# Optimization experiments

Measured on AMD Instinct MI355X. Metric: run time of the kernel, lower is better.

The kernel has to match this reference:

```python
import jax, jax.numpy as jnp
import numpy as np

B, H, N, D = 2, 16, 4096, 128
SCALE = 1.0


def setup_inputs() -> dict:
    key = jax.random.key(0)
    kq, kk, kv, kg = jax.random.split(key, 4)
    shape = (B, H, N, D)
    return {
        "q": jax.random.normal(kq, shape, dtype=jnp.float32),
        "k": jax.random.normal(kk, shape, dtype=jnp.float32),
        "v": jax.random.normal(kv, shape, dtype=jnp.float32),
        "g": jax.random.normal(kg, shape, dtype=jnp.float32),
    }


def reference(q, k, v, g):
    # FLAOperator(mode='gla') CPU fallback: gla_scan
    # recurrence: s_t = s_{t-1} + sigmoid(q_t*k_t + g_t) * v_t ; y_t = s_t
    qs = q * SCALE
    # move time axis (N) to the front for lax.scan: [N, B, H, D]
    seq = tuple(jnp.moveaxis(t, 2, 0) for t in (qs, k, v, g))
    s0 = jnp.zeros((q.shape[0], q.shape[1], q.shape[3]), dtype=q.dtype)  # [B, H, D]

    def step(s, xs):
        q_t, k_t, v_t, g_t = xs
        s = s + jax.nn.sigmoid(q_t * k_t + g_t) * v_t
        return s, s

    _, y = jax.lax.scan(step, s0, seq)  # y: [N, B, H, D]
    return jnp.moveaxis(y, 0, 2)  # [B, H, N, D]
```

## Files before the change

### kernel.cpp

```cpp
#include <hip/hip_runtime.h>
#include <math.h>

static constexpr int kN   = 4096;
static constexpr int kD   = 128;
static constexpr int kBH  = 32;
static constexpr int kD4  = 32;

typedef float  v4f __attribute__((ext_vector_type(4)));

__device__ __forceinline__ float fast_sigmoid(float x) {
    return __builtin_amdgcn_rcpf(1.0f + __expf(-x));
}

__device__ __forceinline__ unsigned short f2b(float x) {
    union { float f; unsigned u; } cv; cv.f = x;
    unsigned u = cv.u;
    u += 0x7fffu + ((u >> 16) & 1u);
    return (unsigned short)(u >> 16);
}
__device__ __forceinline__ float b2f(unsigned short b) {
    union { unsigned u; float f; } cv; cv.u = ((unsigned)b) << 16;
    return cv.f;
}

static constexpr int C1 = 512;
static constexpr int T1 = kN / C1;
static constexpr int TASKS1 = kBH * C1;

__global__ __launch_bounds__(256) void gla1_scan(
    const float4* __restrict__ q, const float4* __restrict__ k,
    const float4* __restrict__ v, const float4* __restrict__ g,
    ushort4* __restrict__ wscan, float4* __restrict__ sums)
{
    const int gtid = blockIdx.x * 256 + threadIdx.x;
    const int lane = gtid & (kD4 - 1);
    const int task = gtid >> 5;
    const int bh   = task >> 9;
    const int c    = task & (C1 - 1);

    const size_t base = ((size_t)bh * kN + (size_t)c * T1) * kD4 + lane;
    float4 acc = make_float4(0.f, 0.f, 0.f, 0.f);
#pragma unroll
    for (int t = 0; t < T1; ++t) {
        const size_t idx = base + (size_t)t * kD4;
        const float4 q4 = q[idx];
        const float4 k4 = k[idx];
        const float4 g4 = g[idx];
        const float4 v4 = v[idx];
        acc.x += v4.x * fast_sigmoid(q4.x * k4.x + g4.x);
        acc.y += v4.y * fast_sigmoid(q4.y * k4.y + g4.y);
        acc.z += v4.z * fast_sigmoid(q4.z * k4.z + g4.z);
        acc.w += v4.w * fast_sigmoid(q4.w * k4.w + g4.w);
        ushort4 p;
        p.x = f2b(acc.x); p.y = f2b(acc.y); p.z = f2b(acc.z); p.w = f2b(acc.w);
        wscan[idx] = p;
    }
    sums[(size_t)task * kD4 + lane] = acc;
}

__global__ void gla1_chunkscan(float* __restrict__ sums)
{
    const int bh = blockIdx.x;
    const int d  = threadIdx.x;
    const size_t base = (size_t)bh * C1 * kD + d;
    float run = 0.f;
    for (int c0 = 0; c0 < C1; c0 += 8) {
        float tv[8];
#pragma unroll
        for (int j = 0; j < 8; ++j)
            tv[j] = sums[base + (size_t)(c0 + j) * kD];
#pragma unroll
        for (int j = 0; j < 8; ++j) {
            const float t = tv[j];
            sums[base + (size_t)(c0 + j) * kD] = run;
            run += t;
        }
    }
}

__global__ __launch_bounds__(256) void gla1_emit(
    const ushort4* __restrict__ wscan, const float4* __restrict__ sums,
    float4* __restrict__ out)
{
    const int gtid = blockIdx.x * 256 + threadIdx.x;
    const int lane = gtid & (kD4 - 1);
    const int task = gtid >> 5;
    const int bh   = task >> 9;
    const int c    = task & (C1 - 1);

    const float4 pre = sums[(size_t)task * kD4 + lane];
    const size_t base = ((size_t)bh * kN + (size_t)c * T1) * kD4 + lane;
#pragma unroll
    for (int t = 0; t < T1; ++t) {
        const size_t idx = base + (size_t)t * kD4;
        const ushort4 p = wscan[idx];
        v4f o;
        o.x = b2f(p.x) + pre.x;
        o.y = b2f(p.y) + pre.y;
        o.z = b2f(p.z) + pre.z;
        o.w = b2f(p.w) + pre.w;
        __builtin_nontemporal_store(o, (v4f*)&out[idx]);
    }
}

template <int CC>
__global__ __launch_bounds__(256) void gla_pass1(
    const float4* __restrict__ q, const float4* __restrict__ k,
    const float4* __restrict__ v, const float4* __restrict__ g,
    float4* __restrict__ out, float4* __restrict__ sums)
{
    constexpr int TT = kN / CC;
    const int gtid = blockIdx.x * 256 + threadIdx.x;
    const int lane = gtid & (kD4 - 1);
    const int task = gtid >> 5;
    const int bh   = task / CC;
    const int c    = task & (CC - 1);
    size_t base = ((size_t)bh * kN + (size_t)c * TT) * kD4 + lane;
    float4 acc = make_float4(0.f, 0.f, 0.f, 0.f);
#pragma unroll 4
    for (int t = 0; t < TT; ++t) {
        const size_t idx = base + (size_t)t * kD4;
        const float4 q4 = q[idx], k4 = k[idx], g4 = g[idx], v4 = v[idx];
        acc.x += v4.x * fast_sigmoid(q4.x * k4.x + g4.x);
        acc.y += v4.y * fast_sigmoid(q4.y * k4.y + g4.y);
        acc.z += v4.z * fast_sigmoid(q4.z * k4.z + g4.z);
        acc.w += v4.w * fast_sigmoid(q4.w * k4.w + g4.w);
        out[idx] = acc;
    }
    sums[(size_t)task * kD4 + lane] = acc;
}

template <int CC>
__global__ void gla_pass2(float* __restrict__ sums)
{
    const int bh = blockIdx.x;
    const int d  = threadIdx.x;
    size_t base = (size_t)bh * CC * kD + d;
    float run = 0.f;
#pragma unroll
    for (int c2 = 0; c2 < CC; ++c2) {
        const size_t i = base + (size_t)c2 * kD;
        const float t = sums[i];
        sums[i] = run;
        run += t;
    }
}

template <int CC>
__global__ __launch_bounds__(256) void gla_pass3(
    float4* __restrict__ out, const float4* __restrict__ sums)
{
    constexpr int TT = kN / CC;
    const int gtid = blockIdx.x * 256 + threadIdx.x;
    const int lane = gtid & (kD4 - 1);
    const int nt   = gtid >> 5;
    const int bh   = nt / kN;
    const int t    = nt & (kN - 1);
    const int c    = t / TT;
    const float4 add = sums[((size_t)bh * CC + c) * kD4 + lane];
    float4 o = out[gtid];
    o.x += add.x; o.y += add.y; o.z += add.z; o.w += add.w;
    out[gtid] = o;
}

extern "C" void kernel_launch(void* const* d_in, const int* in_sizes, int n_in,
                              void* d_out, int out_size, void* d_ws,
                              size_t ws_size, hipStream_t stream)
{
    const float4* q = (const float4*)d_in[0];
    const float4* k = (const float4*)d_in[1];
    const float4* v = (const float4*)d_in[2];
    const float4* g = (const float4*)d_in[3];
    float4* out = (float4*)d_out;

    constexpr size_t kWscanBytes = (size_t)kBH * kN * kD4 * sizeof(ushort4);
    constexpr size_t kSumsBytes  = (size_t)TASKS1 * kD4 * sizeof(float4);
    constexpr size_t kNeed1 = kWscanBytes + kSumsBytes;

    if (ws_size >= kNeed1) {
        ushort4* wscan = (ushort4*)d_ws;
        float4*  sums  = (float4*)((char*)d_ws + kWscanBytes);
        const int blocks = TASKS1 * 32 / 256;
        gla1_scan<<<blocks, 256, 0, stream>>>(q, k, v, g, wscan, sums);
        gla1_chunkscan<<<kBH, kD, 0, stream>>>((float*)sums);
        gla1_emit<<<blocks, 256, 0, stream>>>(wscan, sums, out);
    } else if (ws_size >= (size_t)kBH * 128 * kD * sizeof(float)) {
        constexpr int CC = 128;
        const int threads1 = kBH * CC * 32;
        gla_pass1<CC><<<threads1 / 256, 256, 0, stream>>>(q, k, v, g, out,
                                                          (float4*)d_ws);
        gla_pass2<CC><<<kBH, kD, 0, stream>>>((float*)d_ws);
        const int threads3 = kBH * kN * kD4;
        gla_pass3<CC><<<threads3 / 256, 256, 0, stream>>>(out,
                                                          (const float4*)d_ws);
    } else {
        constexpr int CC = 32;
        const int threads1 = kBH * CC * 32;
        gla_pass1<CC><<<threads1 / 256, 256, 0, stream>>>(q, k, v, g, out,
                                                          (float4*)d_ws);
        gla_pass2<CC><<<kBH, kD, 0, stream>>>((float*)d_ws);
        const int threads3 = kBH * kN * kD4;
        gla_pass3<CC><<<threads3 / 256, 256, 0, stream>>>(out,
                                                          (const float4*)d_ws);
    }
}
```

Baseline: 81.55 us.

## Replace serial chunk-sum scan with hierarchical block-reduced macro scan

The scan kernel now also reduces its 8 chunk sums per block through shared memory into a per-block macro sum. A short 64-step macro scan and a new parallel per-block prefix kernel replace the old 512-step serial chunk scan that ran on only 32 blocks. The emit kernel also preloads all of its bf16 partials before storing. This shortens the serial critical path but adds one extra kernel launch, a __syncthreads, and a small amount of extra workspace traffic.

```diff
diff --git a/kernel.cpp b/kernel.cpp
--- a/kernel.cpp
+++ b/kernel.cpp
@@ -26,19 +26,25 @@
 static constexpr int C1 = 512;
 static constexpr int T1 = kN / C1;
 static constexpr int TASKS1 = kBH * C1;
+static constexpr int M1 = 64;
 
 __global__ __launch_bounds__(256) void gla1_scan(
     const float4* __restrict__ q, const float4* __restrict__ k,
     const float4* __restrict__ v, const float4* __restrict__ g,
-    ushort4* __restrict__ wscan, float4* __restrict__ sums)
-{
+    ushort4* __restrict__ wscan, float4* __restrict__ sums,
+    float4* __restrict__ macros)
+{
+    __shared__ float4 lds[8][kD4];
+
     const int gtid = blockIdx.x * 256 + threadIdx.x;
     const int lane = gtid & (kD4 - 1);
     const int task = gtid >> 5;
     const int bh   = task >> 9;
     const int c    = task & (C1 - 1);
+    const int grp  = threadIdx.x >> 5;
 
     const size_t base = ((size_t)bh * kN + (size_t)c * T1) * kD4 + lane;
+
     float4 acc = make_float4(0.f, 0.f, 0.f, 0.f);
 #pragma unroll
     for (int t = 0; t < T1; ++t) {
@@ -56,25 +62,59 @@
         wscan[idx] = p;
     }
     sums[(size_t)task * kD4 + lane] = acc;
-}
-
-__global__ void gla1_chunkscan(float* __restrict__ sums)
+    lds[grp][lane] = acc;
+    __syncthreads();
+
+    if (threadIdx.x < kD4) {
+        float4 s = lds[0][threadIdx.x];
+#pragma unroll
+        for (int g2 = 1; g2 < 8; ++g2) {
+            const float4 a = lds[g2][threadIdx.x];
+            s.x += a.x; s.y += a.y; s.z += a.z; s.w += a.w;
+        }
+        macros[(size_t)blockIdx.x * kD4 + threadIdx.x] = s;
+    }
+}
+
+__global__ void gla1_macroscan(float* __restrict__ M)
 {
     const int bh = blockIdx.x;
     const int d  = threadIdx.x;
-    const size_t base = (size_t)bh * C1 * kD + d;
+    const size_t base = (size_t)bh * M1 * kD + d;
     float run = 0.f;
-    for (int c0 = 0; c0 < C1; c0 += 8) {
-        float tv[8];
-#pragma unroll
-        for (int j = 0; j < 8; ++j)
-            tv[j] = sums[base + (size_t)(c0 + j) * kD];
-#pragma unroll
-        for (int j = 0; j < 8; ++j) {
+    for (int m0 = 0; m0 < M1; m0 += 16) {
+        float tv[16];
+#pragma unroll
+        for (int j = 0; j < 16; ++j)
+            tv[j] = M[base + (size_t)(m0 + j) * kD];
+#pragma unroll
+        for (int j = 0; j < 16; ++j) {
             const float t = tv[j];
-            sums[base + (size_t)(c0 + j) * kD] = run;
+            M[base + (size_t)(m0 + j) * kD] = run;
             run += t;
         }
+    }
+}
+
+__global__ __launch_bounds__(128) void gla1_chunkpre(
+    float* __restrict__ S, const float* __restrict__ M)
+{
+    const int b  = blockIdx.x;
+    const int d  = threadIdx.x;
+    const int bh = b >> 6;
+    const int m  = b & (M1 - 1);
+    const size_t sbase = ((size_t)bh * C1 + (size_t)m * 8) * kD + d;
+
+    float r[8];
+#pragma unroll
+    for (int j = 0; j < 8; ++j)
+        r[j] = S[sbase + (size_t)j * kD];
+    float pre = M[(size_t)b * kD + d];
+#pragma unroll
+    for (int j = 0; j < 8; ++j) {
+        const float t = r[j];
+        S[sbase + (size_t)j * kD] = pre;
+        pre += t;
     }
 }
 
@@ -88,18 +128,22 @@
     const int bh   = task >> 9;
     const int c    = task & (C1 - 1);
 
+    const size_t base = ((size_t)bh * kN + (size_t)c * T1) * kD4 + lane;
+
+    ushort4 p[T1];
+#pragma unroll
+    for (int t = 0; t < T1; ++t)
+        p[t] = wscan[base + (size_t)t * kD4];
     const float4 pre = sums[(size_t)task * kD4 + lane];
-    const size_t base = ((size_t)bh * kN + (size_t)c * T1) * kD4 + lane;
+
 #pragma unroll
     for (int t = 0; t < T1; ++t) {
-        const size_t idx = base + (size_t)t * kD4;
-        const ushort4 p = wscan[idx];
         v4f o;
-        o.x = b2f(p.x) + pre.x;
-        o.y = b2f(p.y) + pre.y;
-        o.z = b2f(p.z) + pre.z;
-        o.w = b2f(p.w) + pre.w;
-        __builtin_nontemporal_store(o, (v4f*)&out[idx]);
+        o.x = b2f(p[t].x) + pre.x;
+        o.y = b2f(p[t].y) + pre.y;
+        o.z = b2f(p[t].z) + pre.z;
+        o.w = b2f(p[t].w) + pre.w;
+        __builtin_nontemporal_store(o, (v4f*)&out[base + (size_t)t * kD4]);
     }
 }
 
@@ -175,14 +219,18 @@
 
     constexpr size_t kWscanBytes = (size_t)kBH * kN * kD4 * sizeof(ushort4);
     constexpr size_t kSumsBytes  = (size_t)TASKS1 * kD4 * sizeof(float4);
-    constexpr size_t kNeed1 = kWscanBytes + kSumsBytes;
+    constexpr size_t kMacroBytes = (size_t)kBH * M1 * kD4 * sizeof(float4);
+    constexpr size_t kNeed1 = kWscanBytes + kSumsBytes + kMacroBytes;
 
     if (ws_size >= kNeed1) {
         ushort4* wscan = (ushort4*)d_ws;
         float4*  sums  = (float4*)((char*)d_ws + kWscanBytes);
+        float4*  macros= (float4*)((char*)d_ws + kWscanBytes + kSumsBytes);
         const int blocks = TASKS1 * 32 / 256;
-        gla1_scan<<<blocks, 256, 0, stream>>>(q, k, v, g, wscan, sums);
-        gla1_chunkscan<<<kBH, kD, 0, stream>>>((float*)sums);
+        gla1_scan<<<blocks, 256, 0, stream>>>(q, k, v, g, wscan, sums, macros);
+        gla1_macroscan<<<kBH, kD, 0, stream>>>((float*)macros);
+        gla1_chunkpre<<<kBH * M1, kD, 0, stream>>>((float*)sums,
+                                                   (const float*)macros);
         gla1_emit<<<blocks, 256, 0, stream>>>(wscan, sums, out);
     } else if (ws_size >= (size_t)kBH * 128 * kD * sizeof(float)) {
         constexpr int CC = 128;
```

Result: faster. 76.39 us (-6.3%).
